# Optimization experiments

Hardware: AMD Instinct MI355X
Metric: run time of the kernel (lower is better)

## Reference

```python
import jax, jax.numpy as jnp
import numpy as np

H_IMG, W_IMG = 48, 64  # feature-map resolution hard-coded in the module
NUM_HEADS = 8


def get_positional_encodings(B, N, dtype=jnp.float32):
    # (p3^2, p4^2, p3*p4, p3, p4, 1) on normalized grid; intrinsics=None path
    ys = jnp.linspace(-1.0, 1.0, H_IMG, dtype=dtype)
    xs = jnp.linspace(-1.0, 1.0, W_IMG, dtype=dtype)
    p3 = jnp.tile(ys, W_IMG)           # [N] = ys repeated W times (torch repeat)
    p4 = jnp.repeat(xs, H_IMG)         # [N] = each x repeated H times
    pos = jnp.stack([p3 * p3, p4 * p4, p3 * p4, p3, p4, jnp.ones_like(p3)], axis=-1)  # [N,6]
    return jnp.broadcast_to(pos[None], (B, N, 6))


def setup_inputs() -> dict:
    key = jax.random.key(0)
    k1, k2, k3, k4, k5 = jax.random.split(key, 5)
    B, N, C = 2, H_IMG * W_IMG, 256
    s = 0.02
    return {
        "x1": jax.random.normal(k1, (B, N, C), jnp.float32),
        "x2": jax.random.normal(k2, (B, N, C), jnp.float32),
        "Wq": jax.random.normal(k3, (C, C), jnp.float32) * s,      # qkv (one-way: q only)
        "Wkv": jax.random.normal(k4, (C, 2 * C), jnp.float32) * s,  # qkv2 -> k,v
        "Wpf": jax.random.normal(k5, (C + 6 * NUM_HEADS, C), jnp.float32) * s,  # proj_fundamental
        "bpf": jnp.zeros((C,), jnp.float32),
    }


def reference(x1, x2, Wq, Wkv, Wpf, bpf):
    B, N, C = x1.shape
    H = NUM_HEADS
    d = C // H
    scale = d ** -0.5

    # q from x1; k,v from x2 (separate linear, matching torch reshape/permute split)
    q1 = (x1 @ Wq).reshape(B, N, H, d).transpose(0, 2, 1, 3)          # [B,H,N,d]
    kv = (x2 @ Wkv).reshape(B, N, 2, H, d)
    k2 = kv[:, :, 0].transpose(0, 2, 1, 3)                            # [B,H,N,d]
    v2 = kv[:, :, 1].transpose(0, 2, 1, 3)                            # [B,H,N,d]

    attn = jax.nn.softmax(jnp.einsum('bhnd,bhmd->bhnm', q1, k2) * scale, axis=-1)  # [B,H,N,N]

    pos = get_positional_encodings(B, N, x1.dtype)                    # [B,N,6]
    v2p = jnp.concatenate(
        [v2, jnp.broadcast_to(pos[:, None], (B, H, N, 6))], axis=-1)  # [B,H,N,d+6]

    y = jnp.einsum('bhnm,bhmd->bhnd', attn, v2p)                      # [B,H,N,d+6]
    y = y.transpose(0, 2, 1, 3).reshape(B, N, H * (d + 6))            # [B,N,C+6H]
    y = y @ Wpf + bpf                                                 # [B,N,C]
    y = y.reshape(B, N, H, d).transpose(0, 2, 1, 3)                   # [B,H,N,d]

    return jnp.concatenate([attn, y], axis=-1)                        # [B,H,N,N+d]
```

## Files before the change

### kernel.cpp

```cpp
#include <hip/hip_runtime.h>
#include <hip/hip_bf16.h>
#include <cstdint>
#include <cstddef>

#define NB 2
#define NH 8
#define BHN 16
#define NN 3072
#define CC 256
#define DD 32
#define OUTW 3104
#define VW 48
#define KP 384

typedef __attribute__((ext_vector_type(8))) __bf16 bf16x8;
typedef __attribute__((ext_vector_type(4))) short short4v;
typedef __attribute__((ext_vector_type(4))) float f32x4;

static __device__ __forceinline__ unsigned short f2bf(float f) {
    union { float f; unsigned u; } v; v.f = f;
    unsigned r = v.u + 0x7FFFu + ((v.u >> 16) & 1u);
    return (unsigned short)(r >> 16);
}

static __device__ __forceinline__ bf16x8 ldb8(const unsigned short* p) {
    return *(const bf16x8*)p;
}

static __device__ __forceinline__ f32x4 mfma16(bf16x8 a, bf16x8 b, f32x4 c) {
    return __builtin_amdgcn_mfma_f32_16x16x32_bf16(a, b, c, 0, 0, 0);
}

__global__ __launch_bounds__(256) void prep_kernel(
    const float* __restrict__ x1, const float* __restrict__ x2,
    const float* __restrict__ Wq, const float* __restrict__ Wkv,
    const float* __restrict__ Wpf,
    unsigned short* __restrict__ x1b, unsigned short* __restrict__ x2b,
    unsigned short* __restrict__ Wt, unsigned short* __restrict__ Wpft,
    unsigned short* __restrict__ v2pT)
{
    int i = blockIdx.x * 256 + threadIdx.x;
    const int S_X = NB * NN * CC;
    if (i < S_X) { x1b[i] = f2bf(x1[i]); return; }
    i -= S_X;
    if (i < S_X) { x2b[i] = f2bf(x2[i]); return; }
    i -= S_X;
    const int S_WT = 768 * CC;
    if (i < S_WT) {
        int j = i >> 8, kk = i & 255;
        float w = (j < 256) ? Wq[kk * 256 + j] : Wkv[kk * 512 + (j - 256)];
        Wt[i] = f2bf(w);
        return;
    }
    i -= S_WT;
    const int S_WP = 256 * KP;
    if (i < S_WP) {
        int c2 = i / KP, t = i - c2 * KP;
        int h = t / VW, cc = t - h * VW;
        unsigned short v = 0;
        if (cc < 38) v = f2bf(Wpf[(h * 38 + cc) * 256 + c2]);
        Wpft[i] = v;
        return;
    }
    i -= S_WP;
    const int S_POS = BHN * 16 * NN;
    if (i < S_POS) {
        int n = i % NN;
        int r = i / NN;
        int bh = r >> 4;
        int c = (r & 15) + 32;
        float val = 0.f;
        if (c < 38) {
            float p3 = -1.f + 2.f * (float)(n % 48) / 47.f;
            float p4 = -1.f + 2.f * (float)(n / 48) / 63.f;
            float pv[6] = { p3 * p3, p4 * p4, p3 * p4, p3, p4, 1.f };
            val = pv[c - 32];
        }
        v2pT[((size_t)bh * VW + c) * NN + n] = f2bf(val);
    }
}

__global__ __launch_bounds__(256) void qkv_kernel(
    const unsigned short* __restrict__ x1b, const unsigned short* __restrict__ x2b,
    const unsigned short* __restrict__ Wt,
    unsigned short* __restrict__ qbh, unsigned short* __restrict__ kbh,
    unsigned short* __restrict__ v2pT)
{
    int rt = blockIdx.x, ct = blockIdx.y;
    int wv = threadIdx.x >> 6, lane = threadIdx.x & 63;
    int g = lane >> 4, q = lane & 15;
    int row0 = rt * 64 + wv * 16;
    const unsigned short* A = (ct < 4) ? x1b : x2b;
    const unsigned short* arow = A + (size_t)(row0 + q) * CC + g * 8;
    const unsigned short* brow = Wt + (size_t)(ct * 64 + q) * CC + g * 8;
    f32x4 acc[4];
    #pragma unroll
    for (int cb = 0; cb < 4; ++cb) acc[cb] = f32x4{0.f, 0.f, 0.f, 0.f};
    for (int k0 = 0; k0 < CC; k0 += 32) {
        bf16x8 af = ldb8(arow + k0);
        #pragma unroll
        for (int cb = 0; cb < 4; ++cb)
            acc[cb] = mfma16(af, ldb8(brow + (size_t)cb * 16 * CC + k0), acc[cb]);
    }
    int b = row0 / NN, nb = row0 % NN;
    #pragma unroll
    for (int cb = 0; cb < 4; ++cb) {
        int jj = ct * 64 + cb * 16 + q;
        #pragma unroll
        for (int r = 0; r < 4; ++r) {
            int n = nb + 4 * g + r;
            unsigned short bv = f2bf(acc[cb][r]);
            if (jj < 256) {
                int h = jj >> 5, c = jj & 31;
                qbh[(size_t)((b * NH + h) * NN + n) * DD + c] = bv;
            } else if (jj < 512) {
                int jk = jj - 256; int h = jk >> 5, c = jk & 31;
                kbh[(size_t)((b * NH + h) * NN + n) * DD + c] = bv;
            } else {
                int jv = jj - 512; int h = jv >> 5, c = jv & 31;
                v2pT[(size_t)((b * NH + h) * VW + c) * NN + n] = bv;
            }
        }
    }
}

__global__ __launch_bounds__(256) void attn_kernel(
    const unsigned short* __restrict__ qbh, const unsigned short* __restrict__ kbh,
    const unsigned short* __restrict__ v2pT,
    float* __restrict__ out, unsigned short* __restrict__ yacc)
{
    __shared__ unsigned short plds[4][16][40];
    const float SCALE = 0.17677669529663687f;

    int bh = blockIdx.x;
    int qt = blockIdx.y;
    int wv = threadIdx.x >> 6, lane = threadIdx.x & 63;
    int g = lane >> 4, q = lane & 15;
    int qrow = qt * 64 + wv * 16;

    bf16x8 qf = ldb8(qbh + (size_t)(bh * NN + qrow + q) * DD + g * 8);
    const unsigned short* kbase = kbh + (size_t)bh * NN * DD;
    const unsigned short* vbase = v2pT + (size_t)bh * VW * NN;

    float l = 0.f;
    for (int m0 = 0; m0 < NN; m0 += 32) {
        bf16x8 kf0 = ldb8(kbase + (size_t)(m0 + q) * DD + g * 8);
        bf16x8 kf1 = ldb8(kbase + (size_t)(m0 + 16 + q) * DD + g * 8);
        f32x4 z = {0.f, 0.f, 0.f, 0.f};
        f32x4 s0 = mfma16(kf0, qf, z);
        f32x4 s1 = mfma16(kf1, qf, z);
        #pragma unroll
        for (int r = 0; r < 4; ++r)
            l += __expf(s0[r] * SCALE) + __expf(s1[r] * SCALE);
    }
    l += __shfl_xor(l, 16, 64);
    l += __shfl_xor(l, 32, 64);
    float invl = 1.f / l;

    f32x4 yt0 = {0.f,0.f,0.f,0.f}, yt1 = yt0, yt2 = yt0;
    float* orow = out + (size_t)(bh * NN + qrow + q) * OUTW;
    unsigned short* pl = &plds[wv][q][0];

    for (int m0 = 0; m0 < NN; m0 += 32) {
        bf16x8 kf0 = ldb8(kbase + (size_t)(m0 + q) * DD + g * 8);
        bf16x8 kf1 = ldb8(kbase + (size_t)(m0 + 16 + q) * DD + g * 8);
        f32x4 z = {0.f, 0.f, 0.f, 0.f};
        f32x4 s0 = mfma16(kf0, qf, z);
        f32x4 s1 = mfma16(kf1, qf, z);
        f32x4 p0, p1;
        #pragma unroll
        for (int r = 0; r < 4; ++r) {
            p0[r] = __expf(s0[r] * SCALE) * invl;
            p1[r] = __expf(s1[r] * SCALE) * invl;
        }
        __builtin_nontemporal_store(p0, (f32x4*)(orow + m0 + 4 * g));
        __builtin_nontemporal_store(p1, (f32x4*)(orow + m0 + 16 + 4 * g));
        short4v pk0, pk1;
        #pragma unroll
        for (int r = 0; r < 4; ++r) {
            pk0[r] = (short)f2bf(p0[r]);
            pk1[r] = (short)f2bf(p1[r]);
        }
        *(short4v*)(pl + 4 * g) = pk0;
        *(short4v*)(pl + 16 + 4 * g) = pk1;
        asm volatile("s_waitcnt lgkmcnt(0)" ::: "memory");
        __builtin_amdgcn_sched_barrier(0);
        bf16x8 pf = ldb8(pl + 8 * g);
        bf16x8 vf0 = ldb8(vbase + (size_t)(q) * NN + m0 + g * 8);
        bf16x8 vf1 = ldb8(vbase + (size_t)(16 + q) * NN + m0 + g * 8);
        bf16x8 vf2 = ldb8(vbase + (size_t)(32 + q) * NN + m0 + g * 8);
        yt0 = mfma16(vf0, pf, yt0);
        yt1 = mfma16(vf1, pf, yt1);
        yt2 = mfma16(vf2, pf, yt2);
    }

    int b = bh >> 3, h = bh & 7;
    int nrow = qrow + q;
    unsigned short* yrow = yacc + (size_t)(b * NN + nrow) * KP + h * VW;
    f32x4 yts[3] = { yt0, yt1, yt2 };
    #pragma unroll
    for (int cb = 0; cb < 3; ++cb) {
        short4v pk;
        #pragma unroll
        for (int r = 0; r < 4; ++r) pk[r] = (short)f2bf(yts[cb][r]);
        *(short4v*)(yrow + cb * 16 + 4 * g) = pk;
    }
}

__global__ __launch_bounds__(256) void proj_kernel(
    const unsigned short* __restrict__ yacc, const unsigned short* __restrict__ Wpft,
    const float* __restrict__ bpf, float* __restrict__ out)
{
    int rt = blockIdx.x, ct = blockIdx.y;
    int wv = threadIdx.x >> 6, lane = threadIdx.x & 63;
    int g = lane >> 4, q = lane & 15;
    int row0 = rt * 64 + wv * 16;
    const unsigned short* arow = yacc + (size_t)(row0 + q) * KP + g * 8;
    const unsigned short* b0 = Wpft + (size_t)(ct * 64 + q) * KP + g * 8;
    f32x4 acc[4];
    #pragma unroll
    for (int cb = 0; cb < 4; ++cb) acc[cb] = f32x4{0.f, 0.f, 0.f, 0.f};
    for (int k0 = 0; k0 < KP; k0 += 32) {
        bf16x8 af = ldb8(arow + k0);
        #pragma unroll
        for (int cb = 0; cb < 4; ++cb)
            acc[cb] = mfma16(af, ldb8(b0 + (size_t)cb * 16 * KP + k0), acc[cb]);
    }
    int b = row0 / NN, nb = row0 % NN;
    #pragma unroll
    for (int cb = 0; cb < 4; ++cb) {
        int c2 = ct * 64 + cb * 16 + q;
        float bias = bpf[c2];
        int h = c2 >> 5, c = c2 & 31;
        float* obase = out + (size_t)((b * NH + h) * NN) * OUTW + NN + c;
        #pragma unroll
        for (int r = 0; r < 4; ++r) {
            int n = nb + 4 * g + r;
            __builtin_nontemporal_store(acc[cb][r] + bias, &obase[(size_t)n * OUTW]);
        }
    }
}

extern "C" void kernel_launch(void* const* d_in, const int* in_sizes, int n_in,
                              void* d_out, int out_size, void* d_ws, size_t ws_size,
                              hipStream_t stream)
{
    (void)in_sizes; (void)n_in; (void)out_size; (void)ws_size;
    const float* x1  = (const float*)d_in[0];
    const float* x2  = (const float*)d_in[1];
    const float* Wq  = (const float*)d_in[2];
    const float* Wkv = (const float*)d_in[3];
    const float* Wpf = (const float*)d_in[4];
    const float* bpf = (const float*)d_in[5];
    float* out = (float*)d_out;
    char* ws = (char*)d_ws;

    unsigned short* x1b  = (unsigned short*)(ws + 0);
    unsigned short* x2b  = (unsigned short*)(ws + 3145728);
    unsigned short* Wt   = (unsigned short*)(ws + 6291456);
    unsigned short* Wpft = (unsigned short*)(ws + 6684672);
    unsigned short* qbh  = (unsigned short*)(ws + 6881280);
    unsigned short* kbh  = (unsigned short*)(ws + 10027008);
    unsigned short* v2pT = (unsigned short*)(ws + 13172736);
    unsigned short* yacc = (unsigned short*)(ws + 17891328);

    prep_kernel<<<16512, 256, 0, stream>>>(x1, x2, Wq, Wkv, Wpf, x1b, x2b, Wt, Wpft, v2pT);
    qkv_kernel<<<dim3(96, 12), 256, 0, stream>>>(x1b, x2b, Wt, qbh, kbh, v2pT);
    attn_kernel<<<dim3(16, 48), 256, 0, stream>>>(qbh, kbh, v2pT, out, yacc);
    proj_kernel<<<dim3(96, 4), 256, 0, stream>>>(yacc, Wpft, bpf, out);
}
```

Before: 256.4 us.

## Split attention key range across waves, prefetch K/V, fold normalization into exp2

```diff
diff --git a/kernel.cpp b/kernel.cpp
--- a/kernel.cpp
+++ b/kernel.cpp
@@ -18,9 +18,8 @@
 typedef __attribute__((ext_vector_type(4))) float f32x4;
 
 static __device__ __forceinline__ unsigned short f2bf(float f) {
-    union { float f; unsigned u; } v; v.f = f;
-    unsigned r = v.u + 0x7FFFu + ((v.u >> 16) & 1u);
-    return (unsigned short)(r >> 16);
+    __hip_bfloat16 h = __float2bfloat16(f);
+    return *reinterpret_cast<unsigned short*>(&h);
 }
 
 static __device__ __forceinline__ bf16x8 ldb8(const unsigned short* p) {
@@ -124,57 +123,77 @@
     }
 }
 
-__global__ __launch_bounds__(256) void attn_kernel(
+__global__ __launch_bounds__(256, 4) void attn_kernel(
     const unsigned short* __restrict__ qbh, const unsigned short* __restrict__ kbh,
     const unsigned short* __restrict__ v2pT,
     float* __restrict__ out, unsigned short* __restrict__ yacc)
 {
     __shared__ unsigned short plds[4][16][40];
-    const float SCALE = 0.17677669529663687f;
+    __shared__ float lsum[4][16];
+    __shared__ float yl[4][48][17];
+    const float C = 0.17677669529663687f * 1.4426950408889634f;
 
     int bh = blockIdx.x;
     int qt = blockIdx.y;
     int wv = threadIdx.x >> 6, lane = threadIdx.x & 63;
     int g = lane >> 4, q = lane & 15;
-    int qrow = qt * 64 + wv * 16;
+    int qrow = qt * 16;
+    int mbase = wv * 768;
 
     bf16x8 qf = ldb8(qbh + (size_t)(bh * NN + qrow + q) * DD + g * 8);
     const unsigned short* kbase = kbh + (size_t)bh * NN * DD;
     const unsigned short* vbase = v2pT + (size_t)bh * VW * NN;
 
     float l = 0.f;
-    for (int m0 = 0; m0 < NN; m0 += 32) {
-        bf16x8 kf0 = ldb8(kbase + (size_t)(m0 + q) * DD + g * 8);
-        bf16x8 kf1 = ldb8(kbase + (size_t)(m0 + 16 + q) * DD + g * 8);
-        f32x4 z = {0.f, 0.f, 0.f, 0.f};
-        f32x4 s0 = mfma16(kf0, qf, z);
-        f32x4 s1 = mfma16(kf1, qf, z);
-        #pragma unroll
-        for (int r = 0; r < 4; ++r)
-            l += __expf(s0[r] * SCALE) + __expf(s1[r] * SCALE);
+    {
+        bf16x8 kf0 = ldb8(kbase + (size_t)(mbase + q) * DD + g * 8);
+        bf16x8 kf1 = ldb8(kbase + (size_t)(mbase + 16 + q) * DD + g * 8);
+        for (int it = 0; it < 24; ++it) {
+            int m0 = mbase + it * 32;
+            bf16x8 kn0 = ldb8(kbase + (size_t)(m0 + 32 + q) * DD + g * 8);
+            bf16x8 kn1 = ldb8(kbase + (size_t)(m0 + 48 + q) * DD + g * 8);
+            f32x4 z = {0.f, 0.f, 0.f, 0.f};
+            f32x4 s0 = mfma16(kf0, qf, z);
+            f32x4 s1 = mfma16(kf1, qf, z);
+            #pragma unroll
+            for (int r = 0; r < 4; ++r)
+                l += exp2f(s0[r] * C) + exp2f(s1[r] * C);
+            kf0 = kn0; kf1 = kn1;
+        }
     }
     l += __shfl_xor(l, 16, 64);
     l += __shfl_xor(l, 32, 64);
-    float invl = 1.f / l;
+    if (lane < 16) lsum[wv][q] = l;
+    __syncthreads();
+    float ltot = lsum[0][q] + lsum[1][q] + lsum[2][q] + lsum[3][q];
+    float nl2 = -__log2f(ltot);
 
     f32x4 yt0 = {0.f,0.f,0.f,0.f}, yt1 = yt0, yt2 = yt0;
     float* orow = out + (size_t)(bh * NN + qrow + q) * OUTW;
     unsigned short* pl = &plds[wv][q][0];
 
-    for (int m0 = 0; m0 < NN; m0 += 32) {
-        bf16x8 kf0 = ldb8(kbase + (size_t)(m0 + q) * DD + g * 8);
-        bf16x8 kf1 = ldb8(kbase + (size_t)(m0 + 16 + q) * DD + g * 8);
+    bf16x8 kf0 = ldb8(kbase + (size_t)(mbase + q) * DD + g * 8);
+    bf16x8 kf1 = ldb8(kbase + (size_t)(mbase + 16 + q) * DD + g * 8);
+    for (int it = 0; it < 24; ++it) {
+        int m0 = mbase + it * 32;
+        bf16x8 kn0 = ldb8(kbase + (size_t)(m0 + 32 + q) * DD + g * 8);
+        bf16x8 kn1 = ldb8(kbase + (size_t)(m0 + 48 + q) * DD + g * 8);
+        bf16x8 vf0 = ldb8(vbase + (size_t)(q) * NN + m0 + g * 8);
+        bf16x8 vf1 = ldb8(vbase + (size_t)(16 + q) * NN + m0 + g * 8);
+        bf16x8 vf2 = ldb8(vbase + (size_t)(32 + q) * NN + m0 + g * 8);
+
         f32x4 z = {0.f, 0.f, 0.f, 0.f};
         f32x4 s0 = mfma16(kf0, qf, z);
         f32x4 s1 = mfma16(kf1, qf, z);
         f32x4 p0, p1;
         #pragma unroll
         for (int r = 0; r < 4; ++r) {
-            p0[r] = __expf(s0[r] * SCALE) * invl;
-            p1[r] = __expf(s1[r] * SCALE) * invl;
+            p0[r] = exp2f(__builtin_fmaf(s0[r], C, nl2));
+            p1[r] = exp2f(__builtin_fmaf(s1[r], C, nl2));
         }
         __builtin_nontemporal_store(p0, (f32x4*)(orow + m0 + 4 * g));
         __builtin_nontemporal_store(p1, (f32x4*)(orow + m0 + 16 + 4 * g));
+
         short4v pk0, pk1;
         #pragma unroll
         for (int r = 0; r < 4; ++r) {
@@ -186,23 +205,32 @@
         asm volatile("s_waitcnt lgkmcnt(0)" ::: "memory");
         __builtin_amdgcn_sched_barrier(0);
         bf16x8 pf = ldb8(pl + 8 * g);
-        bf16x8 vf0 = ldb8(vbase + (size_t)(q) * NN + m0 + g * 8);
-        bf16x8 vf1 = ldb8(vbase + (size_t)(16 + q) * NN + m0 + g * 8);
-        bf16x8 vf2 = ldb8(vbase + (size_t)(32 + q) * NN + m0 + g * 8);
         yt0 = mfma16(vf0, pf, yt0);
         yt1 = mfma16(vf1, pf, yt1);
         yt2 = mfma16(vf2, pf, yt2);
-    }
-
-    int b = bh >> 3, h = bh & 7;
-    int nrow = qrow + q;
-    unsigned short* yrow = yacc + (size_t)(b * NN + nrow) * KP + h * VW;
-    f32x4 yts[3] = { yt0, yt1, yt2 };
-    #pragma unroll
-    for (int cb = 0; cb < 3; ++cb) {
+        kf0 = kn0; kf1 = kn1;
+    }
+
+    {
+        f32x4 yts[3] = { yt0, yt1, yt2 };
+        #pragma unroll
+        for (int cb = 0; cb < 3; ++cb)
+            #pragma unroll
+            for (int r = 0; r < 4; ++r)
+                yl[wv][cb * 16 + 4 * g + r][q] = yts[cb][r];
+    }
+    __syncthreads();
+    if (wv < 3) {
+        int cb = wv;
+        int b = bh >> 3, h = bh & 7;
+        unsigned short* yrow = yacc + (size_t)(b * NN + qrow + q) * KP + h * VW;
         short4v pk;
         #pragma unroll
-        for (int r = 0; r < 4; ++r) pk[r] = (short)f2bf(yts[cb][r]);
+        for (int r = 0; r < 4; ++r) {
+            int c = cb * 16 + 4 * g + r;
+            float s = yl[0][c][q] + yl[1][c][q] + yl[2][c][q] + yl[3][c][q];
+            pk[r] = (short)f2bf(s);
+        }
         *(short4v*)(yrow + cb * 16 + 4 * g) = pk;
     }
 }
@@ -266,6 +294,6 @@
 
     prep_kernel<<<16512, 256, 0, stream>>>(x1, x2, Wq, Wkv, Wpf, x1b, x2b, Wt, Wpft, v2pT);
     qkv_kernel<<<dim3(96, 12), 256, 0, stream>>>(x1b, x2b, Wt, qbh, kbh, v2pT);
-    attn_kernel<<<dim3(16, 48), 256, 0, stream>>>(qbh, kbh, v2pT, out, yacc);
+    attn_kernel<<<dim3(16, 192), 256, 0, stream>>>(qbh, kbh, v2pT, out, yacc);
     proj_kernel<<<dim3(96, 4), 256, 0, stream>>>(yacc, Wpft, bpf, out);
 }
```

Result: no change. 253.3 us (-1.2%).

## Stage softmax tiles in swizzled LDS for coalesced attn writes and prefetch K/V

Applied to the files above, without the earlier changes.

```diff
diff --git a/kernel.cpp b/kernel.cpp
--- a/kernel.cpp
+++ b/kernel.cpp
@@ -18,9 +18,8 @@
 typedef __attribute__((ext_vector_type(4))) float f32x4;
 
 static __device__ __forceinline__ unsigned short f2bf(float f) {
-    union { float f; unsigned u; } v; v.f = f;
-    unsigned r = v.u + 0x7FFFu + ((v.u >> 16) & 1u);
-    return (unsigned short)(r >> 16);
+    __hip_bfloat16 h = __float2bfloat16(f);
+    return *reinterpret_cast<unsigned short*>(&h);
 }
 
 static __device__ __forceinline__ bf16x8 ldb8(const unsigned short* p) {
@@ -29,6 +28,13 @@
 
 static __device__ __forceinline__ f32x4 mfma16(bf16x8 a, bf16x8 b, f32x4 c) {
     return __builtin_amdgcn_mfma_f32_16x16x32_bf16(a, b, c, 0, 0, 0);
+}
+
+static __device__ __forceinline__ float bfhi2f(unsigned u) {
+    union { unsigned u; float f; } v; v.u = u & 0xffff0000u; return v.f;
+}
+static __device__ __forceinline__ float bflo2f(unsigned u) {
+    union { unsigned u; float f; } v; v.u = u << 16; return v.f;
 }
 
 __global__ __launch_bounds__(256) void prep_kernel(
@@ -129,8 +135,8 @@
     const unsigned short* __restrict__ v2pT,
     float* __restrict__ out, unsigned short* __restrict__ yacc)
 {
-    __shared__ unsigned short plds[4][16][40];
-    const float SCALE = 0.17677669529663687f;
+    __shared__ unsigned short ptile[4][16][256];
+    const float C = 0.17677669529663687f * 1.4426950408889634f;
 
     int bh = blockIdx.x;
     int qt = blockIdx.y;
@@ -143,55 +149,77 @@
     const unsigned short* vbase = v2pT + (size_t)bh * VW * NN;
 
     float l = 0.f;
-    for (int m0 = 0; m0 < NN; m0 += 32) {
-        bf16x8 kf0 = ldb8(kbase + (size_t)(m0 + q) * DD + g * 8);
-        bf16x8 kf1 = ldb8(kbase + (size_t)(m0 + 16 + q) * DD + g * 8);
-        f32x4 z = {0.f, 0.f, 0.f, 0.f};
-        f32x4 s0 = mfma16(kf0, qf, z);
-        f32x4 s1 = mfma16(kf1, qf, z);
-        #pragma unroll
-        for (int r = 0; r < 4; ++r)
-            l += __expf(s0[r] * SCALE) + __expf(s1[r] * SCALE);
+    {
+        bf16x8 kf0 = ldb8(kbase + (size_t)(q) * DD + g * 8);
+        bf16x8 kf1 = ldb8(kbase + (size_t)(16 + q) * DD + g * 8);
+        for (int it = 0; it < 96; ++it) {
+            int m0 = it * 32;
+            bf16x8 kn0 = ldb8(kbase + (size_t)(m0 + 32 + q) * DD + g * 8);
+            bf16x8 kn1 = ldb8(kbase + (size_t)(m0 + 48 + q) * DD + g * 8);
+            f32x4 z = {0.f, 0.f, 0.f, 0.f};
+            f32x4 s0 = mfma16(kf0, qf, z);
+            f32x4 s1 = mfma16(kf1, qf, z);
+            #pragma unroll
+            for (int r = 0; r < 4; ++r)
+                l += exp2f(s0[r] * C) + exp2f(s1[r] * C);
+            kf0 = kn0; kf1 = kn1;
+        }
     }
     l += __shfl_xor(l, 16, 64);
     l += __shfl_xor(l, 32, 64);
-    float invl = 1.f / l;
+    float nl2 = -__log2f(l);
 
     f32x4 yt0 = {0.f,0.f,0.f,0.f}, yt1 = yt0, yt2 = yt0;
-    float* orow = out + (size_t)(bh * NN + qrow + q) * OUTW;
-    unsigned short* pl = &plds[wv][q][0];
-
-    for (int m0 = 0; m0 < NN; m0 += 32) {
-        bf16x8 kf0 = ldb8(kbase + (size_t)(m0 + q) * DD + g * 8);
-        bf16x8 kf1 = ldb8(kbase + (size_t)(m0 + 16 + q) * DD + g * 8);
-        f32x4 z = {0.f, 0.f, 0.f, 0.f};
-        f32x4 s0 = mfma16(kf0, qf, z);
-        f32x4 s1 = mfma16(kf1, qf, z);
-        f32x4 p0, p1;
-        #pragma unroll
-        for (int r = 0; r < 4; ++r) {
-            p0[r] = __expf(s0[r] * SCALE) * invl;
-            p1[r] = __expf(s1[r] * SCALE) * invl;
-        }
-        __builtin_nontemporal_store(p0, (f32x4*)(orow + m0 + 4 * g));
-        __builtin_nontemporal_store(p1, (f32x4*)(orow + m0 + 16 + 4 * g));
-        short4v pk0, pk1;
-        #pragma unroll
-        for (int r = 0; r < 4; ++r) {
-            pk0[r] = (short)f2bf(p0[r]);
-            pk1[r] = (short)f2bf(p1[r]);
-        }
-        *(short4v*)(pl + 4 * g) = pk0;
-        *(short4v*)(pl + 16 + 4 * g) = pk1;
-        asm volatile("s_waitcnt lgkmcnt(0)" ::: "memory");
-        __builtin_amdgcn_sched_barrier(0);
-        bf16x8 pf = ldb8(pl + 8 * g);
-        bf16x8 vf0 = ldb8(vbase + (size_t)(q) * NN + m0 + g * 8);
-        bf16x8 vf1 = ldb8(vbase + (size_t)(16 + q) * NN + m0 + g * 8);
-        bf16x8 vf2 = ldb8(vbase + (size_t)(32 + q) * NN + m0 + g * 8);
-        yt0 = mfma16(vf0, pf, yt0);
-        yt1 = mfma16(vf1, pf, yt1);
-        yt2 = mfma16(vf2, pf, yt2);
+    char* myt = (char*)&ptile[wv][0][0];
+    char* prow = myt + q * 512;
+    unsigned swq = (unsigned)((q & 7) << 4);
+
+    bf16x8 kf0 = ldb8(kbase + (size_t)(q) * DD + g * 8);
+    bf16x8 kf1 = ldb8(kbase + (size_t)(16 + q) * DD + g * 8);
+    bf16x8 vf0 = ldb8(vbase + (size_t)(q) * NN + g * 8);
+    bf16x8 vf1 = ldb8(vbase + (size_t)(16 + q) * NN + g * 8);
+    bf16x8 vf2 = ldb8(vbase + (size_t)(32 + q) * NN + g * 8);
+
+    for (int ph = 0; ph < 12; ++ph) {
+        #pragma unroll
+        for (int it2 = 0; it2 < 8; ++it2) {
+            int m0 = ph * 256 + it2 * 32;
+            bf16x8 kn0 = ldb8(kbase + (size_t)(m0 + 32 + q) * DD + g * 8);
+            bf16x8 kn1 = ldb8(kbase + (size_t)(m0 + 48 + q) * DD + g * 8);
+            bf16x8 vn0 = ldb8(vbase + (size_t)(q) * NN + m0 + 32 + g * 8);
+            bf16x8 vn1 = ldb8(vbase + (size_t)(16 + q) * NN + m0 + 32 + g * 8);
+            bf16x8 vn2 = ldb8(vbase + (size_t)(32 + q) * NN + m0 + 32 + g * 8);
+
+            f32x4 z = {0.f, 0.f, 0.f, 0.f};
+            f32x4 s0 = mfma16(kf0, qf, z);
+            f32x4 s1 = mfma16(kf1, qf, z);
+            short4v pk0, pk1;
+            #pragma unroll
+            for (int r = 0; r < 4; ++r) {
+                pk0[r] = (short)f2bf(exp2f(__builtin_fmaf(s0[r], C, nl2)));
+                pk1[r] = (short)f2bf(exp2f(__builtin_fmaf(s1[r], C, nl2)));
+            }
+            unsigned b0 = (unsigned)(it2 * 64 + 8 * g);
+            *(short4v*)(prow + (b0 ^ swq)) = pk0;
+            *(short4v*)(prow + ((b0 + 32) ^ swq)) = pk1;
+            asm volatile("s_waitcnt lgkmcnt(0)" ::: "memory");
+            __builtin_amdgcn_sched_barrier(0);
+            bf16x8 pf = *(const bf16x8*)(prow + ((unsigned)(it2 * 64 + 16 * g) ^ swq));
+            yt0 = mfma16(vf0, pf, yt0);
+            yt1 = mfma16(vf1, pf, yt1);
+            yt2 = mfma16(vf2, pf, yt2);
+            kf0 = kn0; kf1 = kn1; vf0 = vn0; vf1 = vn1; vf2 = vn2;
+        }
+        #pragma unroll
+        for (int i = 0; i < 16; ++i) {
+            unsigned off = ((unsigned)(lane * 8)) ^ ((unsigned)((i & 7) << 4));
+            uint2 d = *(const uint2*)(myt + i * 512 + off);
+            f32x4 v;
+            v[0] = bflo2f(d.x); v[1] = bfhi2f(d.x);
+            v[2] = bflo2f(d.y); v[3] = bfhi2f(d.y);
+            float* dst = out + (size_t)(bh * NN + qrow + i) * OUTW + ph * 256 + lane * 4;
+            __builtin_nontemporal_store(v, (f32x4*)dst);
+        }
     }
 
     int b = bh >> 3, h = bh & 7;
```

Result: faster. 240.9 us (-6.0%).
